# Optimization experiments

Hardware: AMD Instinct MI355X
Metric: run time of the kernel (lower is better)

## Reference

```python
import jax, jax.numpy as jnp
import numpy as np

B, S, D, H, FF = 4, 2048, 768, 12, 3072
DH = D // H
EPS = 1e-5
NEG = -1e18


def setup_inputs() -> dict:
    key = jax.random.key(0)
    ks = jax.random.split(key, 12)
    xavier = lambda k, fi, fo: jax.random.uniform(k, (fi, fo), jnp.float32,
                                                  -np.sqrt(6.0 / (fi + fo)), np.sqrt(6.0 / (fi + fo)))
    return {
        "x": jax.random.normal(ks[0], (B, S, D), jnp.float32),
        "mask": jax.random.bernoulli(ks[1], 0.1, (B, S, S)),  # True = masked
        "wq": xavier(ks[2], D, D),
        "wk": xavier(ks[3], D, D),
        "wv": xavier(ks[4], D, D),
        "wo": xavier(ks[5], D, D),
        "bo": jnp.zeros((D,), jnp.float32),
        "w1": xavier(ks[6], D, FF),
        "w2": xavier(ks[7], FF, D),
        "g1": jnp.ones((D,), jnp.float32),
        "b1": jnp.zeros((D,), jnp.float32),
        "g2": jnp.ones((D,), jnp.float32),
        "b2": jnp.zeros((D,), jnp.float32),
    }


def _layernorm(x, g, b):
    mu = jnp.mean(x, axis=-1, keepdims=True)
    var = jnp.mean(jnp.square(x - mu), axis=-1, keepdims=True)
    return (x - mu) * jax.lax.rsqrt(var + EPS) * g + b


def reference(x, mask, wq, wk, wv, wo, bo, w1, w2, g1, b1, g2, b2):
    # --- self-attention sublayer (pre-LN) ---
    h = _layernorm(x, g1, b1)
    split = lambda t: t.reshape(B, S, H, DH).transpose(0, 2, 1, 3)  # [B,H,S,DH]
    q = split(h @ wq) / np.sqrt(DH)
    k = split(h @ wk)
    v = split(h @ wv)
    scores = jnp.einsum('bhqd,bhkd->bhqk', q, k)
    scores = jnp.where(mask[:, None, :, :], NEG, scores)
    weights = jax.nn.softmax(scores, axis=-1)
    ctx = jnp.einsum('bhqk,bhkd->bhqd', weights, v)
    ctx = ctx.transpose(0, 2, 1, 3).reshape(B, S, D)
    x = x + (ctx @ wo + bo)
    # --- feed-forward sublayer (pre-LN) ---
    h = _layernorm(x, g2, b2)
    y = jax.nn.relu(h @ w1) @ w2
    return x + y
```

## Files before the change

kernel.cpp:

```cpp
#include <hip/hip_runtime.h>
#include <cstdint>


typedef __bf16 bf16_t;
typedef __bf16 bf16x8 __attribute__((ext_vector_type(8)));
typedef __bf16 bf16x4 __attribute__((ext_vector_type(4)));
typedef __bf16 bf16x2 __attribute__((ext_vector_type(2)));
typedef float  f32x4  __attribute__((ext_vector_type(4)));
typedef float  f32x16 __attribute__((ext_vector_type(16)));

#define LOG2E 1.44269504088896340736f

__device__ __forceinline__ float exp2_fast(float x) {
  float r;
  asm("v_exp_f32 %0, %1" : "=v"(r) : "v"(x));
  return r;
}

__device__ __forceinline__ f32x4 mfma16(bf16x8 a, bf16x8 b, f32x4 c) {
  return __builtin_amdgcn_mfma_f32_16x16x32_bf16(a, b, c, 0, 0, 0);
}
__device__ __forceinline__ f32x16 mfma32(bf16x8 a, bf16x8 b, f32x16 c) {
  return __builtin_amdgcn_mfma_f32_32x32x16_bf16(a, b, c, 0, 0, 0);
}

__device__ __forceinline__ void gload16(const bf16_t* gsrc, bf16_t* lds) {
  __builtin_amdgcn_global_load_lds(
      (const __attribute__((address_space(1))) unsigned int*)(uintptr_t)gsrc,
      (__attribute__((address_space(3))) unsigned int*)(uintptr_t)lds,
      16, 0, 0);
}

__device__ __forceinline__ unsigned pk2(float a, float b) {
  bf16x2 v = {(bf16_t)a, (bf16_t)b};
  return __builtin_bit_cast(unsigned, v);
}
__device__ __forceinline__ void pl32_swap(unsigned& a, unsigned& b) {
  asm("v_permlane32_swap_b32 %0, %1" : "+v"(a), "+v"(b));
}
__device__ __forceinline__ bf16x8 frag4(unsigned w0, unsigned w1,
                                        unsigned w2, unsigned w3) {
  union { unsigned u[4]; bf16x8 v; } t;
  t.u[0] = w0; t.u[1] = w1; t.u[2] = w2; t.u[3] = w3;
  return t.v;
}

__global__ __launch_bounds__(256) void prep_all(
    const float* __restrict__ wq, const float* __restrict__ wk,
    const float* __restrict__ wv, const float* __restrict__ wo,
    const float* __restrict__ w1, const float* __restrict__ w2,
    bf16_t* __restrict__ dst,
    const int* __restrict__ mask, unsigned int* __restrict__ bits,
    const float* __restrict__ x, const float* __restrict__ g1,
    const float* __restrict__ b1, bf16_t* __restrict__ hout)
{
  const int t = threadIdx.y * 32 + threadIdx.x;
  if (blockIdx.x >= 23296) {
    const int w = t >> 6, lane = t & 63;
    const int row = (blockIdx.x - 23296) * 4 + w;
    const float* xr = x + (size_t)row * 768;
    float4 v[3];
    float s = 0.f, s2 = 0.f;
#pragma unroll
    for (int p = 0; p < 3; ++p) {
      v[p] = *(const float4*)(xr + p * 256 + lane * 4);
      s  += v[p].x + v[p].y + v[p].z + v[p].w;
      s2 += v[p].x * v[p].x + v[p].y * v[p].y + v[p].z * v[p].z + v[p].w * v[p].w;
    }
#pragma unroll
    for (int m = 1; m <= 32; m <<= 1) {
      s  += __shfl_xor(s, m, 64);
      s2 += __shfl_xor(s2, m, 64);
    }
    const float mu  = s * (1.0f / 768.0f);
    const float var = s2 * (1.0f / 768.0f) - mu * mu;
    const float rs  = rsqrtf(var + 1e-5f);
    bf16_t* orow = hout + (size_t)row * 768;
#pragma unroll
    for (int p = 0; p < 3; ++p) {
      const float4 g4 = *(const float4*)(g1 + p * 256 + lane * 4);
      const float4 b4 = *(const float4*)(b1 + p * 256 + lane * 4);
      bf16x4 o = {(bf16_t)((v[p].x - mu) * rs * g4.x + b4.x),
                  (bf16_t)((v[p].y - mu) * rs * g4.y + b4.y),
                  (bf16_t)((v[p].z - mu) * rs * g4.z + b4.z),
                  (bf16_t)((v[p].w - mu) * rs * g4.w + b4.w)};
      *(bf16x4*)(orow + p * 256 + lane * 4) = o;
    }
    return;
  }
  if (blockIdx.x >= 6912) {
    const int gid4 = (blockIdx.x - 6912) * 256 + t;
    const int4 v = ((const int4*)mask)[gid4];
    unsigned nib = (v.x != 0 ? 1u : 0u) | (v.y != 0 ? 2u : 0u) |
                   (v.z != 0 ? 4u : 0u) | (v.w != 0 ? 8u : 0u);
    nib <<= ((t & 7) * 4);
    nib |= __shfl_xor((int)nib, 1, 64);
    nib |= __shfl_xor((int)nib, 2, 64);
    nib |= __shfl_xor((int)nib, 4, 64);
    if ((t & 7) == 0) bits[gid4 >> 3] = nib;
    return;
  }
  __shared__ float tile[32][33];
  const int id = blockIdx.x;
  const float* W; size_t doff; int K, N, tx, local; float scale = 1.f;
  if (id < 576)       { W = wq; doff = 0;       K = 768;  N = 768;  tx = 24; local = id;        scale = 0.125f * LOG2E; }
  else if (id < 1152) { W = wk; doff = 589824;  K = 768;  N = 768;  tx = 24; local = id - 576;  }
  else if (id < 1728) { W = wv; doff = 1179648; K = 768;  N = 768;  tx = 24; local = id - 1152; }
  else if (id < 2304) { W = wo; doff = 1769472; K = 768;  N = 768;  tx = 24; local = id - 1728; }
  else if (id < 4608) { W = w1; doff = 2359296; K = 768;  N = 3072; tx = 96; local = id - 2304; }
  else                { W = w2; doff = 4718592; K = 3072; N = 768;  tx = 24; local = id - 4608; }
  const int n0 = (local % tx) * 32, k0 = (local / tx) * 32;
  const int tx_ = threadIdx.x, ty_ = threadIdx.y;
#pragma unroll
  for (int i = 0; i < 32; i += 8)
    tile[ty_ + i][tx_] = W[(size_t)(k0 + ty_ + i) * N + n0 + tx_];
  __syncthreads();
  bf16_t* const Wt = dst + doff;
#pragma unroll
  for (int i = 0; i < 32; i += 8)
    Wt[(size_t)(n0 + ty_ + i) * K + k0 + tx_] = (bf16_t)(tile[tx_][ty_ + i] * scale);
}

__global__ __launch_bounds__(256) void ln_kernel(
    const float* __restrict__ xin, const float* __restrict__ gamma,
    const float* __restrict__ beta, bf16_t* __restrict__ outb)
{
  const int w = threadIdx.x >> 6, lane = threadIdx.x & 63;
  const int row = blockIdx.x * 4 + w;
  const float* xr = xin + (size_t)row * 768;
  float4 v[3];
  float s = 0.f, s2 = 0.f;
#pragma unroll
  for (int p = 0; p < 3; ++p) {
    v[p] = *(const float4*)(xr + p * 256 + lane * 4);
    s  += v[p].x + v[p].y + v[p].z + v[p].w;
    s2 += v[p].x * v[p].x + v[p].y * v[p].y + v[p].z * v[p].z + v[p].w * v[p].w;
  }
#pragma unroll
  for (int m = 1; m <= 32; m <<= 1) {
    s  += __shfl_xor(s, m, 64);
    s2 += __shfl_xor(s2, m, 64);
  }
  const float mu  = s * (1.0f / 768.0f);
  const float var = s2 * (1.0f / 768.0f) - mu * mu;
  const float rs  = rsqrtf(var + 1e-5f);
  bf16_t* orow = outb + (size_t)row * 768;
#pragma unroll
  for (int p = 0; p < 3; ++p) {
    const float4 g4 = *(const float4*)(gamma + p * 256 + lane * 4);
    const float4 b4 = *(const float4*)(beta  + p * 256 + lane * 4);
    bf16x4 o = {(bf16_t)((v[p].x - mu) * rs * g4.x + b4.x),
                (bf16_t)((v[p].y - mu) * rs * g4.y + b4.y),
                (bf16_t)((v[p].z - mu) * rs * g4.z + b4.z),
                (bf16_t)((v[p].w - mu) * rs * g4.w + b4.w)};
    *(bf16x4*)(orow + p * 256 + lane * 4) = o;
  }
}

template <bool RELU, bool OUT_F32, bool HAS_BIAS, bool HAS_RES, bool VOUT, int BNT>
__global__ __launch_bounds__(256) void gemm_kernel(
    const bf16_t* __restrict__ A, const bf16_t* __restrict__ Bt,
    void* __restrict__ Cout, const float* __restrict__ bias,
    const float* __restrict__ res, int Mdim, int Ndim, int Kdim,
    bf16_t* __restrict__ vout)
{
  constexpr int WCW = BNT / 2;
  constexpr int NJ  = WCW / 16;
  __shared__ __align__(16) bf16_t Smem[2 * (128 + BNT) * 64];
  const int tid = threadIdx.x;
  const int lane = tid & 63, w = tid >> 6;
  const int l15 = lane & 15, g = lane >> 4;
  const int gx = gridDim.x;
  const int nwg = gx * gridDim.y;
  const int p = blockIdx.y * gx + blockIdx.x;
  const int wg = (p & 7) * (nwg >> 3) + (p >> 3);
  const int bm = (wg / gx) * 128, bn = (wg % gx) * BNT;
  const int wr = (w >> 1) * 64, wc = (w & 1) * WCW;
  const int swz = l15 & 7;

  auto STAGE = [&](int kt, int buf) {
    const int k0 = kt << 6;
    bf16_t* const as = Smem + buf * (128 + BNT) * 64;
    bf16_t* const bs = as + 128 * 64;
#pragma unroll
    for (int it = 0; it < 4; ++it) {
      const int ch = it * 256 + tid;
      const int r = ch >> 3, c = ch & 7;
      gload16(A + (size_t)(bm + r) * Kdim + k0 + ((c ^ (r & 7)) * 8), as + ch * 8);
    }
#pragma unroll
    for (int it = 0; it < BNT / 32; ++it) {
      const int ch = it * 256 + tid;
      const int r = ch >> 3, c = ch & 7;
      gload16(Bt + (size_t)(bn + r) * Kdim + k0 + ((c ^ (r & 7)) * 8), bs + ch * 8);
    }
  };

  f32x4 acc[4][NJ] = {};
  const int nK = Kdim >> 6;
  STAGE(0, 0);
  __syncthreads();
  for (int kt = 0; kt < nK; ++kt) {
    const int cur = kt & 1;
    if (kt + 1 < nK) STAGE(kt + 1, cur ^ 1);
    const bf16_t* const As = Smem + cur * (128 + BNT) * 64;
    const bf16_t* const Bs = As + 128 * 64;
#pragma unroll
    for (int kk = 0; kk < 2; ++kk) {
      bf16x8 af[4], bfr[NJ];
#pragma unroll
      for (int i = 0; i < 4; ++i)
        af[i] = *(const bf16x8*)(As + (wr + i * 16 + l15) * 64 +
                                 (((kk * 4 + g) ^ swz) * 8));
#pragma unroll
      for (int j = 0; j < NJ; ++j)
        bfr[j] = *(const bf16x8*)(Bs + (wc + j * 16 + l15) * 64 +
                                  (((kk * 4 + g) ^ swz) * 8));
#pragma unroll
      for (int i = 0; i < 4; ++i)
#pragma unroll
        for (int j = 0; j < NJ; ++j)
          acc[i][j] = mfma16(af[i], bfr[j], acc[i][j]);
    }
    __syncthreads();
  }

  if constexpr (!OUT_F32) {
    bf16_t* const wb = Smem + w * 4096;
    if (VOUT && bn >= 1536) {
#pragma unroll
      for (int i = 0; i < 4; ++i)
#pragma unroll
        for (int j = 0; j < NJ; ++j)
#pragma unroll
          for (int r = 0; r < 4; ++r) {
            const int srow = i * 16 + g * 4 + r;
            const int d = j * 16 + l15;
            *(bf16_t*)((char*)wb + d * 128 + ((srow * 2) ^ ((d & 7) << 4))) =
                (bf16_t)acc[i][j][r];
          }
      __syncthreads();
      const int b = bm >> 11;
      const int h = (bn + wc - 1536) >> 6;
      const int s0 = (bm & 2047) + wr;
      const int c = lane & 7;
#pragma unroll
      for (int ps = 0; ps < 8; ++ps) {
        const int drow = (lane >> 3) + ps * 8;
        bf16x8 v = *(const bf16x8*)((char*)wb + drow * 128 +
                                    ((c * 16) ^ ((drow & 7) << 4)));
        *(bf16x8*)(vout + ((size_t)((b * 12 + h) * 64 + drow)) * 2048 +
                   s0 + c * 8) = v;
      }
    } else {
#pragma unroll
      for (int i = 0; i < 4; ++i)
#pragma unroll
        for (int j = 0; j < NJ; ++j)
#pragma unroll
          for (int r = 0; r < 4; ++r) {
            const int row = i * 16 + g * 4 + r, col = j * 16 + l15;
            float v = acc[i][j][r];
            if constexpr (RELU) v = fmaxf(v, 0.f);
            *(bf16_t*)((char*)wb + row * 128 + ((col * 2) ^ ((row & 7) << 4))) =
                (bf16_t)v;
          }
      __syncthreads();
      bf16_t* const crow0 = (bf16_t*)Cout + (size_t)(bm + wr) * Ndim + bn + wc;
      const int c = lane & 7;
#pragma unroll
      for (int ps = 0; ps < 8; ++ps) {
        const int row = (lane >> 3) + ps * 8;
        bf16x8 v = *(const bf16x8*)((char*)wb + row * 128 +
                                    ((c * 16) ^ ((row & 7) << 4)));
        *(bf16x8*)(crow0 + (size_t)row * Ndim + c * 8) = v;
      }
    }
  } else {
    float* const fb = (float*)Smem + w * 2048;
    const int c = lane & 7;
#pragma unroll
    for (int jh = 0; jh < WCW / 32; ++jh) {
      if (jh) __syncthreads();
#pragma unroll
      for (int i = 0; i < 4; ++i)
#pragma unroll
        for (int jj = 0; jj < 2; ++jj)
#pragma unroll
          for (int r = 0; r < 4; ++r) {
            const int row = i * 16 + g * 4 + r, col = jj * 16 + l15;
            *(float*)((char*)fb + row * 128 + ((col * 4) ^ ((row & 7) << 4))) =
                acc[i][jh * 2 + jj][r];
          }
      __syncthreads();
      const int gcol = bn + wc + jh * 32 + c * 4;
      float4 bv = {0.f, 0.f, 0.f, 0.f};
      if constexpr (HAS_BIAS) bv = *(const float4*)(bias + gcol);
#pragma unroll
      for (int ps = 0; ps < 8; ++ps) {
        const int row = (lane >> 3) + ps * 8;
        float4 v = *(const float4*)((char*)fb + row * 128 +
                                    ((c * 16) ^ ((row & 7) << 4)));
        if constexpr (HAS_BIAS) { v.x += bv.x; v.y += bv.y; v.z += bv.z; v.w += bv.w; }
        if constexpr (HAS_RES) {
          const float4 rv = *(const float4*)(res + (size_t)(bm + wr + row) * Ndim + gcol);
          v.x += rv.x; v.y += rv.y; v.z += rv.z; v.w += rv.w;
        }
        *(float4*)((float*)Cout + (size_t)(bm + wr + row) * Ndim + gcol) = v;
      }
    }
  }
}

__global__ __launch_bounds__(256, 4) void attn_kernel(
    const bf16_t* __restrict__ qkv, const bf16_t* __restrict__ vT,
    const unsigned int* __restrict__ mbits, bf16_t* __restrict__ ctx)
{
  __shared__ __align__(16) bf16_t KsBuf[2][64 * 64];
  __shared__ __align__(16) bf16_t VsBuf[2][64 * 64];
  const int tid = threadIdx.x;
  const int lane = tid & 63, w = tid >> 6;
  const int q32 = lane & 31, hi = lane >> 5;
  const int bh = blockIdx.x;
  const int qt = blockIdx.y;
  const int b = bh / 12, h = bh % 12;
  const int qabs = qt * 128 + w * 32 + q32;

  bf16x8 qf[4];
#pragma unroll
  for (int c = 0; c < 4; ++c)
    qf[c] = *(const bf16x8*)(qkv + (size_t)(b * 2048 + qabs) * 2304 +
                             h * 64 + c * 16 + hi * 8);

  auto stage = [&](bf16_t* ks, bf16_t* vs, int kt) {
    const size_t kb0 = (size_t)(b * 2048 + kt * 64);
#pragma unroll
    for (int it = 0; it < 2; ++it) {
      const int ch = it * 256 + tid;
      const int r = ch >> 3, c = ch & 7;
      gload16(qkv + (kb0 + r) * 2304 + 768 + h * 64 + ((c ^ (r & 7)) * 8), ks + ch * 8);
    }
#pragma unroll
    for (int it = 0; it < 2; ++it) {
      const int ch = it * 256 + tid;
      const int r = ch >> 3, c = ch & 7;
      gload16(vT + (size_t)(bh * 64 + r) * 2048 + kt * 64 + ((c ^ (r & 7)) * 8),
              vs + ch * 8);
    }
  };

  f32x16 oacc[2] = {};
  float lr0 = 0.f, lr1 = 0.f, lr2 = 0.f, lr3 = 0.f;

  stage(KsBuf[0], VsBuf[0], 0);
  __syncthreads();

  for (int kt = 0; kt < 32; ++kt) {
    const bf16_t* ksc = (kt & 1) ? KsBuf[1] : KsBuf[0];
    const bf16_t* vsc = (kt & 1) ? VsBuf[1] : VsBuf[0];
    if (kt < 31)
      stage((kt & 1) ? KsBuf[0] : KsBuf[1], (kt & 1) ? VsBuf[0] : VsBuf[1], kt + 1);

    const uint2 mm = *(const uint2*)(mbits + (size_t)(b * 2048 + qabs) * 64 + kt * 2);
    const unsigned mwv[2] = {mm.x >> (hi * 4), mm.y >> (hi * 4)};

    f32x16 sacc[2] = {};
#pragma unroll
    for (int c = 0; c < 4; ++c) {
#pragma unroll
      for (int kb = 0; kb < 2; ++kb) {
        const int row = kb * 32 + q32;
        const int slot = (2 * c + hi) ^ (row & 7);
        bf16x8 kf = *(const bf16x8*)(ksc + row * 64 + slot * 8);
        sacc[kb] = mfma32(kf, qf[c], sacc[kb]);
      }
    }

#pragma unroll
    for (int kb = 0; kb < 2; ++kb) {
#pragma unroll
      for (int rq = 0; rq < 4; ++rq) {
        const unsigned sel = mwv[kb] >> (8 * rq);
        {
          const float e0 = exp2_fast(sacc[kb][rq * 4 + 0]);
          const float p0 = (sel & 1u) ? 0.f : e0;
          sacc[kb][rq * 4 + 0] = p0;  lr0 += p0;
          const float e1 = exp2_fast(sacc[kb][rq * 4 + 1]);
          const float p1 = ((sel >> 1) & 1u) ? 0.f : e1;
          sacc[kb][rq * 4 + 1] = p1;  lr1 += p1;
          const float e2 = exp2_fast(sacc[kb][rq * 4 + 2]);
          const float p2 = ((sel >> 2) & 1u) ? 0.f : e2;
          sacc[kb][rq * 4 + 2] = p2;  lr2 += p2;
          const float e3 = exp2_fast(sacc[kb][rq * 4 + 3]);
          const float p3 = ((sel >> 3) & 1u) ? 0.f : e3;
          sacc[kb][rq * 4 + 3] = p3;  lr3 += p3;
        }
      }
    }

    __builtin_amdgcn_s_setprio(1);
#pragma unroll
    for (int kb = 0; kb < 2; ++kb) {
      unsigned u0 = pk2(sacc[kb][0],  sacc[kb][1]);
      unsigned u1 = pk2(sacc[kb][2],  sacc[kb][3]);
      unsigned u2 = pk2(sacc[kb][4],  sacc[kb][5]);
      unsigned u3 = pk2(sacc[kb][6],  sacc[kb][7]);
      unsigned u4 = pk2(sacc[kb][8],  sacc[kb][9]);
      unsigned u5 = pk2(sacc[kb][10], sacc[kb][11]);
      unsigned u6 = pk2(sacc[kb][12], sacc[kb][13]);
      unsigned u7 = pk2(sacc[kb][14], sacc[kb][15]);
      pl32_swap(u0, u2);  pl32_swap(u1, u3);
      pl32_swap(u4, u6);  pl32_swap(u5, u7);
      bf16x8 p0 = frag4(u0, u1, u2, u3);
      bf16x8 p1 = frag4(u4, u5, u6, u7);
#pragma unroll
      for (int ks = 0; ks < 2; ++ks) {
        const bf16x8 pf = ks ? p1 : p0;
        const int cg = kb * 4 + ks * 2 + hi;
#pragma unroll
        for (int dt = 0; dt < 2; ++dt) {
          const int row = dt * 32 + q32;
          bf16x8 vf = *(const bf16x8*)(vsc + row * 64 + ((cg ^ (row & 7)) * 8));
          oacc[dt] = mfma32(vf, pf, oacc[dt]);
        }
      }
    }
    __builtin_amdgcn_s_setprio(0);
    __syncthreads();
  }

  float lrun = (lr0 + lr1) + (lr2 + lr3);
  lrun += __shfl_xor(lrun, 32, 64);
  const float inv = (lrun > 0.f) ? 1.f / lrun : 0.f;
  bf16_t* crow = ctx + (size_t)(b * 2048 + qabs) * 768 + h * 64;
#pragma unroll
  for (int dt = 0; dt < 2; ++dt)
#pragma unroll
    for (int rq = 0; rq < 4; ++rq) {
      bf16x4 ov = {(bf16_t)(oacc[dt][rq * 4 + 0] * inv),
                   (bf16_t)(oacc[dt][rq * 4 + 1] * inv),
                   (bf16_t)(oacc[dt][rq * 4 + 2] * inv),
                   (bf16_t)(oacc[dt][rq * 4 + 3] * inv)};
      *(bf16x4*)(crow + dt * 32 + rq * 8 + hi * 4) = ov;
    }
}

extern "C" void kernel_launch(void* const* d_in, const int* in_sizes, int n_in,
                              void* d_out, int out_size, void* d_ws, size_t ws_size,
                              hipStream_t stream) {
  const float* x  = (const float*)d_in[0];
  const int* mask = (const int*)d_in[1];
  const float* wq = (const float*)d_in[2];
  const float* wk = (const float*)d_in[3];
  const float* wv = (const float*)d_in[4];
  const float* wo = (const float*)d_in[5];
  const float* bo = (const float*)d_in[6];
  const float* w1 = (const float*)d_in[7];
  const float* w2 = (const float*)d_in[8];
  const float* g1 = (const float*)d_in[9];
  const float* b1 = (const float*)d_in[10];
  const float* g2 = (const float*)d_in[11];
  const float* b2 = (const float*)d_in[12];
  float* out = (float*)d_out;

  char* p = (char*)d_ws;
  bf16_t* WQKVT = (bf16_t*)p; p += (size_t)2304 * 768 * 2;
  bf16_t* WOT   = (bf16_t*)p; p += (size_t)768 * 768 * 2;
  bf16_t* W1T   = (bf16_t*)p; p += (size_t)3072 * 768 * 2;
  bf16_t* W2T   = (bf16_t*)p; p += (size_t)768 * 3072 * 2;
  unsigned int* MB = (unsigned int*)p; p += (size_t)4 * 2048 * 64 * 4;
  bf16_t* Hbuf  = (bf16_t*)p; p += (size_t)8192 * 768 * 2;
  float*  X2    = (float*)p;  p += (size_t)8192 * 768 * 4;
  bf16_t* QKV   = (bf16_t*)p; p += (size_t)8192 * 2304 * 2;
  bf16_t* CTX   = (bf16_t*)p;
  bf16_t* FFN   = QKV;
  bf16_t* VT    = (bf16_t*)X2;

  prep_all<<<6912 + 16384 + 2048, dim3(32, 8), 0, stream>>>(
      wq, wk, wv, wo, w1, w2, WQKVT, mask, MB, x, g1, b1, Hbuf);

  gemm_kernel<false, false, false, false, true, 128><<<dim3(18, 64), 256, 0, stream>>>(
      Hbuf, WQKVT, QKV, nullptr, nullptr, 8192, 2304, 768, VT);
  attn_kernel<<<dim3(48, 16), 256, 0, stream>>>(QKV, VT, MB, CTX);
  gemm_kernel<false, true, true, true, false, 64><<<dim3(12, 64), 256, 0, stream>>>(
      CTX, WOT, X2, bo, x, 8192, 768, 768, nullptr);

  ln_kernel<<<2048, 256, 0, stream>>>(X2, g2, b2, Hbuf);
  gemm_kernel<true, false, false, false, false, 128><<<dim3(24, 64), 256, 0, stream>>>(
      Hbuf, W1T, FFN, nullptr, nullptr, 8192, 3072, 768, nullptr);
  gemm_kernel<false, true, false, true, false, 64><<<dim3(12, 64), 256, 0, stream>>>(
      FFN, W2T, out, nullptr, X2, 8192, 768, 3072, nullptr);
}
```

Measured before the change: 254.8 us.

## Switch GEMM mainloop to 3-stage BK=32 pipeline with partial vmcnt waits

The GEMM main loop goes from a double-buffered K-tile of 64 to a triple-buffered K-tile of 32, with loads issued two stages ahead. Each iteration now waits with a partial s_waitcnt vmcnt on only the oldest stage plus a raw s_barrier, not a full __syncthreads. The goal is to keep more global loads in flight and hide memory latency behind MFMA work. The cost is twice as many iterations and barriers, a 4-wide swizzle that may raise LDS bank conflicts, and hand-tuned vmcnt counts that must match the exact number of loads issued per stage.

Result: slower. 286.8 us (+12.6%).

```diff
diff --git a/kernel.cpp b/kernel.cpp
--- a/kernel.cpp
+++ b/kernel.cpp
@@ -164,9 +164,10 @@
     const float* __restrict__ res, int Mdim, int Ndim, int Kdim,
     bf16_t* __restrict__ vout)
 {
-  constexpr int WCW = BNT / 2;
-  constexpr int NJ  = WCW / 16;
-  __shared__ __align__(16) bf16_t Smem[2 * (128 + BNT) * 64];
+  constexpr int WCW  = BNT / 2;
+  constexpr int NJ   = WCW / 16;
+  constexpr int BUFE = (128 + BNT) * 32;
+  __shared__ __align__(16) bf16_t Smem[3 * BUFE];
   const int tid = threadIdx.x;
   const int lane = tid & 63, w = tid >> 6;
   const int l15 = lane & 15, g = lane >> 4;
@@ -176,54 +177,68 @@
   const int wg = (p & 7) * (nwg >> 3) + (p >> 3);
   const int bm = (wg / gx) * 128, bn = (wg % gx) * BNT;
   const int wr = (w >> 1) * 64, wc = (w & 1) * WCW;
-  const int swz = l15 & 7;
+  const int swz = l15 & 3;
 
   auto STAGE = [&](int kt, int buf) {
-    const int k0 = kt << 6;
-    bf16_t* const as = Smem + buf * (128 + BNT) * 64;
-    bf16_t* const bs = as + 128 * 64;
-#pragma unroll
-    for (int it = 0; it < 4; ++it) {
+    const int k0 = kt << 5;
+    bf16_t* const as = Smem + buf * BUFE;
+    bf16_t* const bs = as + 128 * 32;
+#pragma unroll
+    for (int it = 0; it < 2; ++it) {
       const int ch = it * 256 + tid;
-      const int r = ch >> 3, c = ch & 7;
-      gload16(A + (size_t)(bm + r) * Kdim + k0 + ((c ^ (r & 7)) * 8), as + ch * 8);
-    }
-#pragma unroll
-    for (int it = 0; it < BNT / 32; ++it) {
+      const int r = ch >> 2, c = ch & 3;
+      gload16(A + (size_t)(bm + r) * Kdim + k0 + ((c ^ (r & 3)) * 8), as + ch * 8);
+    }
+#pragma unroll
+    for (int it = 0; it < BNT / 64; ++it) {
       const int ch = it * 256 + tid;
-      const int r = ch >> 3, c = ch & 7;
-      gload16(Bt + (size_t)(bn + r) * Kdim + k0 + ((c ^ (r & 7)) * 8), bs + ch * 8);
+      const int r = ch >> 2, c = ch & 3;
+      gload16(Bt + (size_t)(bn + r) * Kdim + k0 + ((c ^ (r & 3)) * 8), bs + ch * 8);
     }
   };
+  #define WAIT_SL()                                                        \
+    do {                                                                   \
+      if constexpr (BNT == 128)                                            \
+        asm volatile("s_waitcnt vmcnt(4) lgkmcnt(0)" ::: "memory");        \
+      else                                                                 \
+        asm volatile("s_waitcnt vmcnt(3) lgkmcnt(0)" ::: "memory");        \
+    } while (0)
 
   f32x4 acc[4][NJ] = {};
-  const int nK = Kdim >> 6;
+  const int nK = Kdim >> 5;
   STAGE(0, 0);
+  STAGE(1, 1);
+  WAIT_SL();
+  __builtin_amdgcn_s_barrier();
+  int cur = 0;
+  for (int kt = 0; kt < nK; ++kt) {
+    if (kt + 2 < nK) {
+      int nx = cur + 2; if (nx >= 3) nx -= 3;
+      STAGE(kt + 2, nx);
+    }
+    const bf16_t* const As = Smem + cur * BUFE;
+    const bf16_t* const Bs = As + 128 * 32;
+    bf16x8 af[4], bfr[NJ];
+#pragma unroll
+    for (int i = 0; i < 4; ++i)
+      af[i] = *(const bf16x8*)(As + (wr + i * 16 + l15) * 32 + ((g ^ swz) * 8));
+#pragma unroll
+    for (int j = 0; j < NJ; ++j)
+      bfr[j] = *(const bf16x8*)(Bs + (wc + j * 16 + l15) * 32 + ((g ^ swz) * 8));
+#pragma unroll
+    for (int i = 0; i < 4; ++i)
+#pragma unroll
+      for (int j = 0; j < NJ; ++j)
+        acc[i][j] = mfma16(af[i], bfr[j], acc[i][j]);
+    if (kt + 1 < nK) {
+      if (kt + 2 < nK) WAIT_SL();
+      else asm volatile("s_waitcnt vmcnt(0) lgkmcnt(0)" ::: "memory");
+      __builtin_amdgcn_s_barrier();
+    }
+    cur = (cur == 2) ? 0 : cur + 1;
+  }
   __syncthreads();
-  for (int kt = 0; kt < nK; ++kt) {
-    const int cur = kt & 1;
-    if (kt + 1 < nK) STAGE(kt + 1, cur ^ 1);
-    const bf16_t* const As = Smem + cur * (128 + BNT) * 64;
-    const bf16_t* const Bs = As + 128 * 64;
-#pragma unroll
-    for (int kk = 0; kk < 2; ++kk) {
-      bf16x8 af[4], bfr[NJ];
-#pragma unroll
-      for (int i = 0; i < 4; ++i)
-        af[i] = *(const bf16x8*)(As + (wr + i * 16 + l15) * 64 +
-                                 (((kk * 4 + g) ^ swz) * 8));
-#pragma unroll
-      for (int j = 0; j < NJ; ++j)
-        bfr[j] = *(const bf16x8*)(Bs + (wc + j * 16 + l15) * 64 +
-                                  (((kk * 4 + g) ^ swz) * 8));
-#pragma unroll
-      for (int i = 0; i < 4; ++i)
-#pragma unroll
-        for (int j = 0; j < NJ; ++j)
-          acc[i][j] = mfma16(af[i], bfr[j], acc[i][j]);
-    }
-    __syncthreads();
-  }
+  #undef WAIT_SL
 
   if constexpr (!OUT_F32) {
     bf16_t* const wb = Smem + w * 4096;
```
